# Kernel tuning notes

Measured on AMD Instinct MI355X. Metric: run time of the kernel, lower is better.

The kernel has to match this reference:

```python
import jax, jax.numpy as jnp
import numpy as np

VOCAB, D, BLOCK = 32000, 1024, 2048
B, S = 4, 2048

def setup_inputs() -> dict:
    key = jax.random.key(0)
    ks = jax.random.split(key, 12)
    s = 0.02
    return {
        "x": jax.random.randint(ks[0], (B, S), 0, VOCAB),
        "tok_emb": jax.random.normal(ks[1], (VOCAB, D), jnp.float32) * s,
        "pos_emb": jax.random.normal(ks[2], (BLOCK, D), jnp.float32) * s,
        "Wq": jax.random.normal(ks[3], (D, D), jnp.float32) * s,
        "bq": jnp.zeros((D,), jnp.float32),
        "Wk": jax.random.normal(ks[4], (D, D), jnp.float32) * s,
        "bk": jnp.zeros((D,), jnp.float32),
        "Wv": jax.random.normal(ks[5], (D, D), jnp.float32) * s,
        "bv": jnp.zeros((D,), jnp.float32),
        "Wfc": jax.random.normal(ks[6], (VOCAB, D), jnp.float32) * s,
        "bfc": jnp.zeros((VOCAB,), jnp.float32),
    }

def reference(x, tok_emb, pos_emb, Wq, bq, Wk, bk, Wv, bv, Wfc, bfc):
    # embeddings: token lookup + learned positional
    h = tok_emb[x] + pos_emb[jnp.arange(x.shape[1])][None, :, :]  # [B,S,D]
    Q = h @ Wq.T + bq
    K = h @ Wk.T + bk
    V = h @ Wv.T + bv
    scale = 1.0 / jnp.sqrt(jnp.float32(Q.shape[-1]))
    scores = jnp.einsum('bqd,bkd->bqk', Q, K) * scale  # [B,S,S]
    attn = jax.nn.softmax(scores, axis=-1)
    out = jnp.einsum('bqk,bkd->bqd', attn, V)
    return out @ Wfc.T + bfc  # [B,S,VOCAB]
```

## Files before the change

### kernel.cpp

```cpp
#include <hip/hip_runtime.h>
#include <hip/hip_bf16.h>
#include <stdint.h>

typedef __bf16 bf16x8 __attribute__((ext_vector_type(8)));
typedef float f32x4 __attribute__((ext_vector_type(4)));
typedef unsigned short u16x8 __attribute__((ext_vector_type(8)));

#define DEVINL static __device__ __forceinline__

DEVINL unsigned short f2bf(float f) {
  unsigned u = __builtin_bit_cast(unsigned, f);
  unsigned r = (u + 0x7FFFu + ((u >> 16) & 1u)) >> 16;
  return (unsigned short)r;
}
DEVINL float bf2f(unsigned short u) {
  return __builtin_bit_cast(float, ((unsigned)u) << 16);
}

DEVINL void gload_lds16(const unsigned short* g, unsigned short* l) {
  __builtin_amdgcn_global_load_lds(
      (const __attribute__((address_space(1))) void*)g,
      (__attribute__((address_space(3))) void*)l, 16, 0, 0);
}

__global__ __launch_bounds__(256) void embed_cvtq_kernel(
    const int* __restrict__ x, const float* __restrict__ tok,
    const float* __restrict__ pos, unsigned short* __restrict__ hb,
    const float* __restrict__ wq, const float* __restrict__ wk,
    const float* __restrict__ wv, unsigned short* __restrict__ wqkvb)
{
  if (blockIdx.x >= 8192) {
    const int b = blockIdx.x - 8192;
    for (long i = (long)b * 256 + threadIdx.x; i < 786432; i += 512 * 256) {
      const float* src;
      long off;
      if (i < 262144)      { src = wq; off = i; }
      else if (i < 524288) { src = wk; off = i - 262144; }
      else                 { src = wv; off = i - 524288; }
      float4 v = ((const float4*)src)[off];
      ushort4 o;
      o.x = f2bf(v.x); o.y = f2bf(v.y); o.z = f2bf(v.z); o.w = f2bf(v.w);
      ((ushort4*)wqkvb)[i] = o;
    }
    return;
  }
  const int bs = blockIdx.x;
  const int s  = bs & 2047;
  const long trow = (long)x[bs] * 1024;
  const int d = threadIdx.x * 4;
  const float4 t = *(const float4*)(tok + trow + d);
  const float4 p = *(const float4*)(pos + (long)s * 1024 + d);
  ushort4 o;
  o.x = f2bf(t.x + p.x);
  o.y = f2bf(t.y + p.y);
  o.z = f2bf(t.z + p.z);
  o.w = f2bf(t.w + p.w);
  *(ushort4*)(hb + (long)bs * 1024 + d) = o;
}

template<int OUTMODE>
__global__ __launch_bounds__(256) void gemm_bt(
    const unsigned short* __restrict__ A, const unsigned short* __restrict__ B,
    void* __restrict__ Cout, const float* __restrict__ bias,
    float scale, int M, int N, int K,
    long sA, long sB, long sC, int Mb, long tStride, int mapMode)
{
  __shared__ __align__(16) unsigned short lA[128 * 32];
  __shared__ __align__(16) unsigned short lB[128 * 32];
  const int tid = threadIdx.x, wid = tid >> 6, lane = tid & 63;
  int bx, by, bz;
  if (mapMode == 0) {
    bx = blockIdx.x; by = blockIdx.y; bz = blockIdx.z;
  } else {
    const int bid = blockIdx.x;
    const int g = bid & 7, jj = bid >> 3;
    bz = g >> 1;
    by = (g & 1) * 8 + (jj & 7);
    bx = jj >> 3;
  }
  A += (long)bz * sA;
  B += (long)bz * sB;
  const int bm = by * 128, bn = bx * 128;

  const int c0 = wid * 64 + lane, c1 = c0 + 256;
  const unsigned short* gA0 = A + (long)(bm + (c0 >> 2)) * K + (c0 & 3) * 8;
  const unsigned short* gA1 = A + (long)(bm + (c1 >> 2)) * K + (c1 & 3) * 8;
  const unsigned short* gB0 = B + (long)(bn + (c0 >> 2)) * K + (c0 & 3) * 8;
  const unsigned short* gB1 = B + (long)(bn + (c1 >> 2)) * K + (c1 & 3) * 8;
  unsigned short* lA0 = lA + wid * 512;
  unsigned short* lA1 = lA + 2048 + wid * 512;
  unsigned short* lB0 = lB + wid * 512;
  unsigned short* lB1 = lB + 2048 + wid * 512;

  const int wr = (wid >> 1) * 64, wc = (wid & 1) * 64;
  const int lr = lane & 15, lk = (lane >> 4) * 8;

  f32x4 acc[4][4] = {};
  const int nk = K >> 5;
  for (int kt = 0; kt < nk; ++kt) {
    const int ko = kt << 5;
    gload_lds16(gA0 + ko, lA0);
    gload_lds16(gA1 + ko, lA1);
    gload_lds16(gB0 + ko, lB0);
    gload_lds16(gB1 + ko, lB1);
    __syncthreads();
    bf16x8 af[4], bg[4];
#pragma unroll
    for (int m = 0; m < 4; ++m)
      af[m] = *(const bf16x8*)(const void*)(lA + (wr + m * 16 + lr) * 32 + lk);
#pragma unroll
    for (int n = 0; n < 4; ++n)
      bg[n] = *(const bf16x8*)(const void*)(lB + (wc + n * 16 + lr) * 32 + lk);
#pragma unroll
    for (int m = 0; m < 4; ++m)
#pragma unroll
      for (int n = 0; n < 4; ++n)
        acc[m][n] = __builtin_amdgcn_mfma_f32_16x16x32_bf16(af[m], bg[n],
                                                            acc[m][n], 0, 0, 0);
    __syncthreads();
  }

  const int r0 = bm + wr + ((lane >> 4) << 2);
  const int cbase = bn + wc + lr;
#pragma unroll
  for (int n = 0; n < 4; ++n) {
    const int col = cbase + n * 16;
    const float bv = bias ? bias[col] : 0.f;
#pragma unroll
    for (int m = 0; m < 4; ++m) {
      const int row0 = r0 + m * 16;
      if (OUTMODE == 2) {
        float* C = (float*)Cout + (long)bz * sC;
#pragma unroll
        for (int i = 0; i < 4; ++i)
          C[(long)(row0 + i) * N + col] = acc[m][n][i] * scale + bv;
      } else if (OUTMODE == 0) {
        unsigned short* C = (unsigned short*)Cout + (long)bz * sC;
#pragma unroll
        for (int i = 0; i < 4; ++i)
          C[(long)(row0 + i) * N + col] = f2bf(acc[m][n][i] * scale + bv);
      } else {
        unsigned short* C = (unsigned short*)Cout;
        const int b = row0 / Mb;
        const int srow = row0 - b * Mb;
        ushort4 o;
        o.x = f2bf(acc[m][n][0] * scale + bv);
        o.y = f2bf(acc[m][n][1] * scale + bv);
        o.z = f2bf(acc[m][n][2] * scale + bv);
        o.w = f2bf(acc[m][n][3] * scale + bv);
        *(ushort4*)(C + (long)b * tStride + (long)col * Mb + srow) = o;
      }
    }
  }
}

__global__ __launch_bounds__(256) void scores_cvt_kernel(
    const unsigned short* __restrict__ Qb, const unsigned short* __restrict__ Kb,
    unsigned short* __restrict__ Sc,
    const float* __restrict__ wfc, unsigned short* __restrict__ wfcb)
{
  __shared__ __align__(16) unsigned short lA[128 * 32];
  __shared__ __align__(16) unsigned short lB[128 * 32];
  if (blockIdx.x < 1024) {
    for (long i = (long)blockIdx.x * 256 + threadIdx.x; i < 8192000;
         i += 1024 * 256) {
      float4 v = ((const float4*)wfc)[i];
      ushort4 o;
      o.x = f2bf(v.x); o.y = f2bf(v.y); o.z = f2bf(v.z); o.w = f2bf(v.w);
      ((ushort4*)wfcb)[i] = o;
    }
    return;
  }
  constexpr int K = 1024, N = 2048;
  const int tid = threadIdx.x, wid = tid >> 6, lane = tid & 63;
  const int bid = blockIdx.x - 1024;
  const int g = bid & 7, jj = bid >> 3;
  const int bz = g >> 1;
  const int by = (g & 1) * 8 + (jj & 7);
  const int bx = jj >> 3;
  const unsigned short* A = Qb + (long)bz * (2048L * 1024);
  const unsigned short* B = Kb + (long)bz * (2048L * 1024);
  unsigned short* C = Sc + (long)bz * (2048L * 2048);
  const int bm = by * 128, bn = bx * 128;

  const int c0 = wid * 64 + lane, c1 = c0 + 256;
  const unsigned short* gA0 = A + (long)(bm + (c0 >> 2)) * K + (c0 & 3) * 8;
  const unsigned short* gA1 = A + (long)(bm + (c1 >> 2)) * K + (c1 & 3) * 8;
  const unsigned short* gB0 = B + (long)(bn + (c0 >> 2)) * K + (c0 & 3) * 8;
  const unsigned short* gB1 = B + (long)(bn + (c1 >> 2)) * K + (c1 & 3) * 8;
  unsigned short* lA0 = lA + wid * 512;
  unsigned short* lA1 = lA + 2048 + wid * 512;
  unsigned short* lB0 = lB + wid * 512;
  unsigned short* lB1 = lB + 2048 + wid * 512;

  const int wr = (wid >> 1) * 64, wc = (wid & 1) * 64;
  const int lr = lane & 15, lk = (lane >> 4) * 8;

  f32x4 acc[4][4] = {};
  for (int kt = 0; kt < 32; ++kt) {
    const int ko = kt << 5;
    gload_lds16(gA0 + ko, lA0);
    gload_lds16(gA1 + ko, lA1);
    gload_lds16(gB0 + ko, lB0);
    gload_lds16(gB1 + ko, lB1);
    __syncthreads();
    bf16x8 af[4], bg[4];
#pragma unroll
    for (int m = 0; m < 4; ++m)
      af[m] = *(const bf16x8*)(const void*)(lA + (wr + m * 16 + lr) * 32 + lk);
#pragma unroll
    for (int n = 0; n < 4; ++n)
      bg[n] = *(const bf16x8*)(const void*)(lB + (wc + n * 16 + lr) * 32 + lk);
#pragma unroll
    for (int m = 0; m < 4; ++m)
#pragma unroll
      for (int n = 0; n < 4; ++n)
        acc[m][n] = __builtin_amdgcn_mfma_f32_16x16x32_bf16(af[m], bg[n],
                                                            acc[m][n], 0, 0, 0);
    __syncthreads();
  }

  const int r0 = bm + wr + ((lane >> 4) << 2);
  const int cbase = bn + wc + lr;
#pragma unroll
  for (int n = 0; n < 4; ++n) {
    const int col = cbase + n * 16;
#pragma unroll
    for (int m = 0; m < 4; ++m) {
      const int row0 = r0 + m * 16;
#pragma unroll
      for (int i = 0; i < 4; ++i)
        C[(long)(row0 + i) * N + col] = f2bf(acc[m][n][i] * 0.03125f);
    }
  }
}

__global__ __launch_bounds__(256) void qkv_bt(
    const unsigned short* __restrict__ A, const unsigned short* __restrict__ B,
    unsigned short* __restrict__ Qb, unsigned short* __restrict__ Kb,
    unsigned short* __restrict__ Vt,
    const float* __restrict__ bq, const float* __restrict__ bk,
    const float* __restrict__ bv)
{
  constexpr int K = 1024;
  __shared__ __align__(16) unsigned short lA[128 * 32];
  __shared__ __align__(16) unsigned short lB[128 * 32];
  const int tid = threadIdx.x, wid = tid >> 6, lane = tid & 63;
  const int bid = blockIdx.x;
  const int g = bid & 7, j = bid >> 3;
  const int bm = (g * 8 + (j & 7)) * 128;
  const int bn = (j >> 3) * 128;
  const int sector = bn >> 10;
  const int bnl = bn & 1023;

  const int c0 = wid * 64 + lane, c1 = c0 + 256;
  const unsigned short* gA0 = A + (long)(bm + (c0 >> 2)) * K + (c0 & 3) * 8;
  const unsigned short* gA1 = A + (long)(bm + (c1 >> 2)) * K + (c1 & 3) * 8;
  const unsigned short* gB0 = B + (long)(bn + (c0 >> 2)) * K + (c0 & 3) * 8;
  const unsigned short* gB1 = B + (long)(bn + (c1 >> 2)) * K + (c1 & 3) * 8;
  unsigned short* lA0 = lA + wid * 512;
  unsigned short* lA1 = lA + 2048 + wid * 512;
  unsigned short* lB0 = lB + wid * 512;
  unsigned short* lB1 = lB + 2048 + wid * 512;

  const int wr = (wid >> 1) * 64, wc = (wid & 1) * 64;
  const int lr = lane & 15, lk = (lane >> 4) * 8;

  f32x4 acc[4][4] = {};
  for (int kt = 0; kt < 32; ++kt) {
    const int ko = kt << 5;
    gload_lds16(gA0 + ko, lA0);
    gload_lds16(gA1 + ko, lA1);
    gload_lds16(gB0 + ko, lB0);
    gload_lds16(gB1 + ko, lB1);
    __syncthreads();
    bf16x8 af[4], bg[4];
#pragma unroll
    for (int m = 0; m < 4; ++m)
      af[m] = *(const bf16x8*)(const void*)(lA + (wr + m * 16 + lr) * 32 + lk);
#pragma unroll
    for (int n = 0; n < 4; ++n)
      bg[n] = *(const bf16x8*)(const void*)(lB + (wc + n * 16 + lr) * 32 + lk);
#pragma unroll
    for (int m = 0; m < 4; ++m)
#pragma unroll
      for (int n = 0; n < 4; ++n)
        acc[m][n] = __builtin_amdgcn_mfma_f32_16x16x32_bf16(af[m], bg[n],
                                                            acc[m][n], 0, 0, 0);
    __syncthreads();
  }

  const float* bias = (sector == 0) ? bq : (sector == 1) ? bk : bv;
  const int r0 = bm + wr + ((lane >> 4) << 2);
  const int cbase = bnl + wc + lr;
#pragma unroll
  for (int n = 0; n < 4; ++n) {
    const int col = cbase + n * 16;
    const float bb = bias[col];
#pragma unroll
    for (int m = 0; m < 4; ++m) {
      const int row0 = r0 + m * 16;
      if (sector == 2) {
        const int b = row0 >> 11;
        const int srow = row0 & 2047;
        ushort4 o;
        o.x = f2bf(acc[m][n][0] + bb);
        o.y = f2bf(acc[m][n][1] + bb);
        o.z = f2bf(acc[m][n][2] + bb);
        o.w = f2bf(acc[m][n][3] + bb);
        *(ushort4*)(Vt + (long)b * (1024L * 2048) + (long)col * 2048 + srow) = o;
      } else {
        unsigned short* C = (sector == 0) ? Qb : Kb;
#pragma unroll
        for (int i = 0; i < 4; ++i)
          C[(long)(row0 + i) * 1024 + col] = f2bf(acc[m][n][i] + bb);
      }
    }
  }
}

__global__ __launch_bounds__(256) void softmax_kernel(unsigned short* __restrict__ S)
{
  unsigned short* row = S + (long)blockIdx.x * 2048;
  const int t = threadIdx.x, lane = t & 63, wid = t >> 6;
  __shared__ float redm[4], reds[4];
  u16x8 raw = ((const u16x8*)row)[t];
  float v[8];
#pragma unroll
  for (int j = 0; j < 8; ++j) v[j] = bf2f(raw[j]);
  float mx = v[0];
#pragma unroll
  for (int j = 1; j < 8; ++j) mx = fmaxf(mx, v[j]);
#pragma unroll
  for (int off = 32; off; off >>= 1) mx = fmaxf(mx, __shfl_xor(mx, off, 64));
  if (lane == 0) redm[wid] = mx;
  __syncthreads();
  mx = fmaxf(fmaxf(redm[0], redm[1]), fmaxf(redm[2], redm[3]));
  float s = 0.f;
#pragma unroll
  for (int j = 0; j < 8; ++j) { v[j] = __expf(v[j] - mx); s += v[j]; }
#pragma unroll
  for (int off = 32; off; off >>= 1) s += __shfl_xor(s, off, 64);
  if (lane == 0) reds[wid] = s;
  __syncthreads();
  s = reds[0] + reds[1] + reds[2] + reds[3];
  const float inv = 1.f / s;
  u16x8 o;
#pragma unroll
  for (int j = 0; j < 8; ++j) o[j] = f2bf(v[j] * inv);
  ((u16x8*)row)[t] = o;
}

DEVINL bf16x8 ldfrag(const unsigned short* p, int row, int kx) {
  return *(const bf16x8*)((const char*)p + row * 128 + kx);
}

#define BARSB() do { __builtin_amdgcn_s_barrier(); \
                     __builtin_amdgcn_sched_barrier(0); } while (0)
#define LGK0() asm volatile("s_waitcnt lgkmcnt(0)")
#define VM6()  asm volatile("s_waitcnt vmcnt(6)")

#define MF16(rb, aArr, bArr) do { \
  _Pragma("unroll") for (int m_ = 0; m_ < 4; ++m_) \
  _Pragma("unroll") for (int n_ = 0; n_ < 4; ++n_) \
    acc[(rb) + m_][n_] = __builtin_amdgcn_mfma_f32_16x16x32_bf16( \
        aArr[m_], bArr[n_], acc[(rb) + m_][n_], 0, 0, 0); \
} while (0)

#define STG_A(b, h, gk) do { \
  const char* s_ = srcA + (h) * 262144 + (long)(((gk) & 15)) * 128; \
  gload_lds16((const unsigned short*)(s_ + la0), \
              dA + (b) * 16384 + (h) * 8192 + dO0); \
  gload_lds16((const unsigned short*)(s_ + la1), \
              dA + (b) * 16384 + (h) * 8192 + dO1); } while (0)
#define STG_B(b, h, gk) do { \
  int t_ = (gk) >> 4; if (t_ >= len) t_ = len - 1; \
  const char* s_ = Bbase + ((long)(bnStart + t_) << 19) + \
                   (h) * 262144 + (long)(((gk) & 15)) * 128; \
  gload_lds16((const unsigned short*)(s_ + la0), \
              dB + (b) * 16384 + (h) * 8192 + dO0); \
  gload_lds16((const unsigned short*)(s_ + la1), \
              dB + (b) * 16384 + (h) * 8192 + dO1); } while (0)

#define KTILE(BUF, S1, S2, S3, S4) do { \
  bf16x8 b0_[4], b1_[4], aA_[4], aB_[4], aC_[4], aD_[4]; \
  _Pragma("unroll") for (int n = 0; n < 4; ++n) { \
    b0_[n] = ldfrag(dB + (BUF) * 16384, wn * 64 + n * 16 + lr, kx0); \
    b1_[n] = ldfrag(dB + (BUF) * 16384, wn * 64 + n * 16 + lr, kx1); } \
  _Pragma("unroll") for (int m = 0; m < 4; ++m) \
    aA_[m] = ldfrag(dA + (BUF) * 16384, wm * 128 + m * 16 + lr, kx0); \
  S1; \
  BARSB(); LGK0(); __builtin_amdgcn_s_setprio(1); \
  MF16(0, aA_, b0_); \
  __builtin_amdgcn_s_setprio(0); BARSB(); \
  _Pragma("unroll") for (int m = 0; m < 4; ++m) { \
    aB_[m] = ldfrag(dA + (BUF) * 16384, wm * 128 + (4 + m) * 16 + lr, kx0); \
    aC_[m] = ldfrag(dA + (BUF) * 16384, wm * 128 + (4 + m) * 16 + lr, kx1); } \
  S2; \
  BARSB(); LGK0(); __builtin_amdgcn_s_setprio(1); \
  MF16(4, aB_, b0_); \
  __builtin_amdgcn_s_setprio(0); BARSB(); \
  _Pragma("unroll") for (int m = 0; m < 4; ++m) \
    aD_[m] = ldfrag(dA + (BUF) * 16384, wm * 128 + m * 16 + lr, kx1); \
  S3; \
  BARSB(); LGK0(); __builtin_amdgcn_s_setprio(1); \
  MF16(4, aC_, b1_); \
  __builtin_amdgcn_s_setprio(0); BARSB(); \
  S4; VM6(); \
  BARSB(); LGK0(); __builtin_amdgcn_s_setprio(1); \
  MF16(0, aD_, b1_); \
  __builtin_amdgcn_s_setprio(0); BARSB(); \
} while (0)

__global__ __launch_bounds__(512, 2) void gemm256_fc(
    const unsigned short* __restrict__ A, const unsigned short* __restrict__ B,
    float* __restrict__ C, const float* __restrict__ bias)
{
  constexpr int N = 32000;
  __shared__ __align__(16) unsigned short lds[65536];
  const int tid = threadIdx.x, wid = tid >> 6, lane = tid & 63;
  const int wm = wid >> 2, wn = wid & 3;
  const int lr = lane & 15;
  const int kq = (lane >> 4) << 4;
  const int xr = (lane & 7) << 4;
  const int kx0 = kq ^ xr;
  const int kx1 = (64 | kq) ^ xr;

  const int bid = blockIdx.x;
  const int g = bid & 7;
  const int j = bid >> 3;
  const int bm = g * 4 + (j & 3);
  const int q = j >> 2;
  const int bnStart = (q < 5) ? 16 * q : 80 + (q - 5) * 15;
  const int len = (q < 5) ? 16 : 15;

  const int loff0 = wid * 1024 + lane * 16;
  const int loff1 = loff0 + 8192;
  const int r0 = loff0 >> 7, r1 = loff1 >> 7;
  const int c0 = (loff0 & 127) ^ ((r0 & 7) << 4);
  const int c1 = (loff1 & 127) ^ ((r1 & 7) << 4);
  const long la0 = (long)r0 * 2048 + c0;
  const long la1 = (long)r1 * 2048 + c1;
  const char* srcA = (const char*)A + ((long)bm << 19);
  const char* Bbase = (const char*)B;
  unsigned short* dA = lds;
  unsigned short* dB = lds + 32768;
  const int dO0 = wid * 512, dO1 = 4096 + wid * 512;

  f32x4 acc[8][4] = {};
  float bv[4];
#pragma unroll
  for (int n = 0; n < 4; ++n)
    bv[n] = bias[(long)bnStart * 256 + wn * 64 + n * 16 + lr];

  STG_B(0, 0, 0); STG_B(0, 1, 0); STG_A(0, 0, 0); STG_A(0, 1, 0);
  STG_B(1, 0, 1); STG_B(1, 1, 1); STG_A(1, 0, 1);
  VM6();
  BARSB();

  for (int t = 0; t < len; ++t) {
#pragma unroll 1
    for (int it = 0; it < 8; ++it) {
      const int gk = t * 16 + 2 * it;
      KTILE(0, STG_A(1, 1, gk + 1), STG_B(0, 0, gk + 2), STG_B(0, 1, gk + 2),
            STG_A(0, 0, gk + 2));
      KTILE(1, STG_A(0, 1, gk + 2), STG_B(1, 0, gk + 3), STG_B(1, 1, gk + 3),
            STG_A(1, 0, gk + 3));
    }
    const long bnRow = ((long)bnStart + t) * 256;
    const int q4 = (lane >> 4) * 4;
#pragma unroll
    for (int m = 0; m < 8; ++m) {
      const long row = (long)bm * 256 + wm * 128 + m * 16 + q4;
#pragma unroll
      for (int i = 0; i < 4; ++i) {
        float* orow = C + (row + i) * (long)N;
#pragma unroll
        for (int n = 0; n < 4; ++n)
          __builtin_nontemporal_store(acc[m][n][i] + bv[n],
                                      &orow[bnRow + wn * 64 + n * 16 + lr]);
      }
    }
    VM6();
    const int tn = (t + 1 < len) ? t + 1 : t;
#pragma unroll
    for (int n = 0; n < 4; ++n)
      bv[n] = bias[((long)bnStart + tn) * 256 + wn * 64 + n * 16 + lr];
#pragma unroll
    for (int m = 0; m < 8; ++m)
#pragma unroll
      for (int n = 0; n < 4; ++n)
        acc[m][n] = f32x4{0.f, 0.f, 0.f, 0.f};
  }
}

extern "C" void kernel_launch(void* const* d_in, const int* in_sizes, int n_in,
                              void* d_out, int out_size, void* d_ws, size_t ws_size,
                              hipStream_t stream)
{
  const int*   x   = (const int*)d_in[0];
  const float* tok = (const float*)d_in[1];
  const float* pos = (const float*)d_in[2];
  const float* Wq  = (const float*)d_in[3];
  const float* bq  = (const float*)d_in[4];
  const float* Wk  = (const float*)d_in[5];
  const float* bk  = (const float*)d_in[6];
  const float* Wv  = (const float*)d_in[7];
  const float* bv  = (const float*)d_in[8];
  const float* Wfc = (const float*)d_in[9];
  const float* bfc = (const float*)d_in[10];
  float* out = (float*)d_out;

  char* ws = (char*)d_ws;
  unsigned short* hb   = (unsigned short*)(ws);
  unsigned short* Wqb  = (unsigned short*)(ws + 16777216);
  unsigned short* Wfcb = (unsigned short*)(ws + 23068672);
  unsigned short* Qb   = (unsigned short*)(ws + 88604672);
  unsigned short* Kb   = (unsigned short*)(ws + 105381888);
  unsigned short* Vt   = (unsigned short*)(ws + 122159104);
  unsigned short* Sc   = (unsigned short*)(ws + 138936320);
  unsigned short* AO   = hb;

  dim3 blk(256);
  embed_cvtq_kernel<<<dim3(8704), blk, 0, stream>>>(x, tok, pos, hb,
                                                    Wq, Wk, Wv, Wqb);
  qkv_bt<<<dim3(1536), blk, 0, stream>>>(hb, Wqb, Qb, Kb, Vt, bq, bk, bv);
  scores_cvt_kernel<<<dim3(2048), blk, 0, stream>>>(Qb, Kb, Sc, Wfc, Wfcb);
  softmax_kernel<<<8192, 256, 0, stream>>>(Sc);
  gemm_bt<0><<<dim3(512), blk, 0, stream>>>(Sc, Vt, AO, nullptr, 1.f,
      2048, 1024, 2048, 2048L * 2048, 1024L * 2048, 2048L * 1024, 0, 0, 1);
  gemm256_fc<<<dim3(256), dim3(512), 0, stream>>>(AO, Wfcb, out, bfc);
}
```

Measured before the change: 753.2 us.

## Replace QKV projection GEMM with pipelined 256x256 persistent kernel

Drops the simple 128x128-tile QKV kernel, which was single-buffered and synchronised on every k-step. QKV now reuses the software-pipelined, LDS-swizzled 256x256 tile machinery from the vocab projection. Each of 256 blocks covers one 256-row stripe and one or two 256-column tiles, then writes Q and K row-major and V transposed, with bias added. The goal is higher MFMA utilisation and more data reuse per tile. The cost is an uneven split: half the blocks do two tiles and half do one.

```diff
diff --git a/kernel.cpp b/kernel.cpp
--- a/kernel.cpp
+++ b/kernel.cpp
@@ -231,90 +231,6 @@
 #pragma unroll
       for (int i = 0; i < 4; ++i)
         C[(long)(row0 + i) * N + col] = f2bf(acc[m][n][i] * 0.03125f);
-    }
-  }
-}
-
-__global__ __launch_bounds__(256) void qkv_bt(
-    const unsigned short* __restrict__ A, const unsigned short* __restrict__ B,
-    unsigned short* __restrict__ Qb, unsigned short* __restrict__ Kb,
-    unsigned short* __restrict__ Vt,
-    const float* __restrict__ bq, const float* __restrict__ bk,
-    const float* __restrict__ bv)
-{
-  constexpr int K = 1024;
-  __shared__ __align__(16) unsigned short lA[128 * 32];
-  __shared__ __align__(16) unsigned short lB[128 * 32];
-  const int tid = threadIdx.x, wid = tid >> 6, lane = tid & 63;
-  const int bid = blockIdx.x;
-  const int g = bid & 7, j = bid >> 3;
-  const int bm = (g * 8 + (j & 7)) * 128;
-  const int bn = (j >> 3) * 128;
-  const int sector = bn >> 10;
-  const int bnl = bn & 1023;
-
-  const int c0 = wid * 64 + lane, c1 = c0 + 256;
-  const unsigned short* gA0 = A + (long)(bm + (c0 >> 2)) * K + (c0 & 3) * 8;
-  const unsigned short* gA1 = A + (long)(bm + (c1 >> 2)) * K + (c1 & 3) * 8;
-  const unsigned short* gB0 = B + (long)(bn + (c0 >> 2)) * K + (c0 & 3) * 8;
-  const unsigned short* gB1 = B + (long)(bn + (c1 >> 2)) * K + (c1 & 3) * 8;
-  unsigned short* lA0 = lA + wid * 512;
-  unsigned short* lA1 = lA + 2048 + wid * 512;
-  unsigned short* lB0 = lB + wid * 512;
-  unsigned short* lB1 = lB + 2048 + wid * 512;
-
-  const int wr = (wid >> 1) * 64, wc = (wid & 1) * 64;
-  const int lr = lane & 15, lk = (lane >> 4) * 8;
-
-  f32x4 acc[4][4] = {};
-  for (int kt = 0; kt < 32; ++kt) {
-    const int ko = kt << 5;
-    gload_lds16(gA0 + ko, lA0);
-    gload_lds16(gA1 + ko, lA1);
-    gload_lds16(gB0 + ko, lB0);
-    gload_lds16(gB1 + ko, lB1);
-    __syncthreads();
-    bf16x8 af[4], bg[4];
-#pragma unroll
-    for (int m = 0; m < 4; ++m)
-      af[m] = *(const bf16x8*)(const void*)(lA + (wr + m * 16 + lr) * 32 + lk);
-#pragma unroll
-    for (int n = 0; n < 4; ++n)
-      bg[n] = *(const bf16x8*)(const void*)(lB + (wc + n * 16 + lr) * 32 + lk);
-#pragma unroll
-    for (int m = 0; m < 4; ++m)
-#pragma unroll
-      for (int n = 0; n < 4; ++n)
-        acc[m][n] = __builtin_amdgcn_mfma_f32_16x16x32_bf16(af[m], bg[n],
-                                                            acc[m][n], 0, 0, 0);
-    __syncthreads();
-  }
-
-  const float* bias = (sector == 0) ? bq : (sector == 1) ? bk : bv;
-  const int r0 = bm + wr + ((lane >> 4) << 2);
-  const int cbase = bnl + wc + lr;
-#pragma unroll
-  for (int n = 0; n < 4; ++n) {
-    const int col = cbase + n * 16;
-    const float bb = bias[col];
-#pragma unroll
-    for (int m = 0; m < 4; ++m) {
-      const int row0 = r0 + m * 16;
-      if (sector == 2) {
-        const int b = row0 >> 11;
-        const int srow = row0 & 2047;
-        ushort4 o;
-        o.x = f2bf(acc[m][n][0] + bb);
-        o.y = f2bf(acc[m][n][1] + bb);
-        o.z = f2bf(acc[m][n][2] + bb);
-        o.w = f2bf(acc[m][n][3] + bb);
-        *(ushort4*)(Vt + (long)b * (1024L * 2048) + (long)col * 2048 + srow) = o;
-      } else {
-        unsigned short* C = (sector == 0) ? Qb : Kb;
-#pragma unroll
-        for (int i = 0; i < 4; ++i)
-          C[(long)(row0 + i) * 1024 + col] = f2bf(acc[m][n][i] + bb);
-      }
     }
   }
 }
@@ -412,19 +328,32 @@
   __builtin_amdgcn_s_setprio(0); BARSB(); \
 } while (0)
 
+#define G256_PRELUDE() \
+  const int tid = threadIdx.x, wid = tid >> 6, lane = tid & 63; \
+  const int wm = wid >> 2, wn = wid & 3; \
+  const int lr = lane & 15; \
+  const int kq = (lane >> 4) << 4; \
+  const int xr = (lane & 7) << 4; \
+  const int kx0 = kq ^ xr; \
+  const int kx1 = (64 | kq) ^ xr; \
+  const int loff0 = wid * 1024 + lane * 16; \
+  const int loff1 = loff0 + 8192; \
+  const int r0 = loff0 >> 7, r1 = loff1 >> 7; \
+  const int c0 = (loff0 & 127) ^ ((r0 & 7) << 4); \
+  const int c1 = (loff1 & 127) ^ ((r1 & 7) << 4); \
+  const long la0 = (long)r0 * 2048 + c0; \
+  const long la1 = (long)r1 * 2048 + c1; \
+  unsigned short* dA = lds; \
+  unsigned short* dB = lds + 32768; \
+  const int dO0 = wid * 512, dO1 = 4096 + wid * 512
+
 __global__ __launch_bounds__(512, 2) void gemm256_fc(
     const unsigned short* __restrict__ A, const unsigned short* __restrict__ B,
     float* __restrict__ C, const float* __restrict__ bias)
 {
   constexpr int N = 32000;
   __shared__ __align__(16) unsigned short lds[65536];
-  const int tid = threadIdx.x, wid = tid >> 6, lane = tid & 63;
-  const int wm = wid >> 2, wn = wid & 3;
-  const int lr = lane & 15;
-  const int kq = (lane >> 4) << 4;
-  const int xr = (lane & 7) << 4;
-  const int kx0 = kq ^ xr;
-  const int kx1 = (64 | kq) ^ xr;
+  G256_PRELUDE();
 
   const int bid = blockIdx.x;
   const int g = bid & 7;
@@ -434,18 +363,8 @@
   const int bnStart = (q < 5) ? 16 * q : 80 + (q - 5) * 15;
   const int len = (q < 5) ? 16 : 15;
 
-  const int loff0 = wid * 1024 + lane * 16;
-  const int loff1 = loff0 + 8192;
-  const int r0 = loff0 >> 7, r1 = loff1 >> 7;
-  const int c0 = (loff0 & 127) ^ ((r0 & 7) << 4);
-  const int c1 = (loff1 & 127) ^ ((r1 & 7) << 4);
-  const long la0 = (long)r0 * 2048 + c0;
-  const long la1 = (long)r1 * 2048 + c1;
   const char* srcA = (const char*)A + ((long)bm << 19);
   const char* Bbase = (const char*)B;
-  unsigned short* dA = lds;
-  unsigned short* dB = lds + 32768;
-  const int dO0 = wid * 512, dO1 = 4096 + wid * 512;
 
   f32x4 acc[8][4] = {};
   float bv[4];
@@ -486,6 +405,90 @@
 #pragma unroll
     for (int n = 0; n < 4; ++n)
       bv[n] = bias[((long)bnStart + tn) * 256 + wn * 64 + n * 16 + lr];
+#pragma unroll
+    for (int m = 0; m < 8; ++m)
+#pragma unroll
+      for (int n = 0; n < 4; ++n)
+        acc[m][n] = f32x4{0.f, 0.f, 0.f, 0.f};
+  }
+}
+
+__global__ __launch_bounds__(512, 2) void gemm256_qkv(
+    const unsigned short* __restrict__ A, const unsigned short* __restrict__ B,
+    unsigned short* __restrict__ Qb, unsigned short* __restrict__ Kb,
+    unsigned short* __restrict__ Vt,
+    const float* __restrict__ bq, const float* __restrict__ bk,
+    const float* __restrict__ bv)
+{
+  __shared__ __align__(16) unsigned short lds[65536];
+  G256_PRELUDE();
+
+  const int bid = blockIdx.x;
+  const int g = bid & 7;
+  const int j = bid >> 3;
+  const int bm = g * 4 + (j & 3);
+  const int q = j >> 2;
+  const int bnStart = (q < 4) ? 2 * q : 8 + (q - 4);
+  const int len = (q < 4) ? 2 : 1;
+
+  const char* srcA = (const char*)A + ((long)bm << 19);
+  const char* Bbase = (const char*)B;
+
+  f32x4 acc[8][4] = {};
+
+  STG_B(0, 0, 0); STG_B(0, 1, 0); STG_A(0, 0, 0); STG_A(0, 1, 0);
+  STG_B(1, 0, 1); STG_B(1, 1, 1); STG_A(1, 0, 1);
+  VM6();
+  BARSB();
+
+  for (int t = 0; t < len; ++t) {
+#pragma unroll 1
+    for (int it = 0; it < 8; ++it) {
+      const int gk = t * 16 + 2 * it;
+      KTILE(0, STG_A(1, 1, gk + 1), STG_B(0, 0, gk + 2), STG_B(0, 1, gk + 2),
+            STG_A(0, 0, gk + 2));
+      KTILE(1, STG_A(0, 1, gk + 2), STG_B(1, 0, gk + 3), STG_B(1, 1, gk + 3),
+            STG_A(1, 0, gk + 3));
+    }
+    const int bnT = bnStart + t;
+    const int sector = bnT >> 2;
+    const int colb = (bnT & 3) * 256;
+    const float* bias_s = (sector == 0) ? bq : (sector == 1) ? bk : bv;
+    const int q4 = (lane >> 4) * 4;
+    if (sector < 2) {
+      unsigned short* C = (sector == 0) ? Qb : Kb;
+#pragma unroll
+      for (int n = 0; n < 4; ++n) {
+        const int col = colb + wn * 64 + n * 16 + lr;
+        const float bb = bias_s[col];
+#pragma unroll
+        for (int m = 0; m < 8; ++m) {
+          const long row = (long)bm * 256 + wm * 128 + m * 16 + q4;
+#pragma unroll
+          for (int i = 0; i < 4; ++i)
+            C[(row + i) * 1024 + col] = f2bf(acc[m][n][i] + bb);
+        }
+      }
+    } else {
+#pragma unroll
+      for (int n = 0; n < 4; ++n) {
+        const int col = colb + wn * 64 + n * 16 + lr;
+        const float bb = bias_s[col];
+#pragma unroll
+        for (int m = 0; m < 8; ++m) {
+          const long row = (long)bm * 256 + wm * 128 + m * 16 + q4;
+          const int b = (int)(row >> 11);
+          const int srow = (int)(row & 2047);
+          ushort4 o;
+          o.x = f2bf(acc[m][n][0] + bb);
+          o.y = f2bf(acc[m][n][1] + bb);
+          o.z = f2bf(acc[m][n][2] + bb);
+          o.w = f2bf(acc[m][n][3] + bb);
+          *(ushort4*)(Vt + (long)b * (1024L * 2048) + (long)col * 2048 + srow) = o;
+        }
+      }
+    }
+    VM6();
 #pragma unroll
     for (int m = 0; m < 8; ++m)
 #pragma unroll
@@ -524,7 +527,8 @@
   dim3 blk(256);
   embed_cvtq_kernel<<<dim3(8704), blk, 0, stream>>>(x, tok, pos, hb,
                                                     Wq, Wk, Wv, Wqb);
-  qkv_bt<<<dim3(1536), blk, 0, stream>>>(hb, Wqb, Qb, Kb, Vt, bq, bk, bv);
+  gemm256_qkv<<<dim3(256), dim3(512), 0, stream>>>(hb, Wqb, Qb, Kb, Vt,
+                                                   bq, bk, bv);
   scores_cvt_kernel<<<dim3(2048), blk, 0, stream>>>(Qb, Kb, Sc, Wfc, Wfcb);
   softmax_kernel<<<8192, 256, 0, stream>>>(Sc);
   gemm_bt<0><<<dim3(512), blk, 0, stream>>>(Sc, Vt, AO, nullptr, 1.f,
```

Result: no change. 749.5 us (median of 2 runs) (-0.5%).
